# Optimization experiments

Measured on AMD Instinct MI355X. Metric: run time of the kernel, lower is better.

Reference implementation:

```python
import jax, jax.numpy as jnp
import numpy as np

N_SAMPLES = 16384
IN_FEATURES = 2048
N_COMPONENTS = 512
MAX_CROSS_TERMS = 512
# With n_components=512, max_cross_terms=512: interaction_depth=2 -> only pairwise
# cross terms, and n_pairwise = min(512*511//2, 512) = 512 (the first 512 pairs in
# lexicographic (i, j), i<j order -- exactly what the chunked torch loops produce).
_pi, _pj = np.triu_indices(N_COMPONENTS, k=1)  # lexicographic row-major order
PAIR_I = jnp.asarray(_pi[:MAX_CROSS_TERMS])
PAIR_J = jnp.asarray(_pj[:MAX_CROSS_TERMS])
SQRT_EPS = 1e-8


def setup_inputs() -> dict:
    key = jax.random.key(0)
    k1, k2 = jax.random.split(key)
    X = jax.random.normal(k1, (N_SAMPLES, IN_FEATURES), dtype=jnp.float32)
    projection = jax.random.normal(k2, (IN_FEATURES, N_COMPONENTS), dtype=jnp.float32) / np.sqrt(N_COMPONENTS)
    return {"X": X, "projection": projection}


def reference(X, projection):
    # Random projection: [N, in] @ [in, C] -> [N, C]
    Xp = X @ projection
    n = X.shape[0]
    bias = jnp.ones((n, 1), dtype=X.dtype)                 # 'bias' chunk
    p1 = Xp                                                # power_1
    p2 = Xp * Xp                                           # power_2
    p3 = p2 * Xp                                           # power_3
    pairs = Xp[:, PAIR_I] * Xp[:, PAIR_J]                  # pairwise cross terms
    sq = jnp.sqrt(jnp.abs(Xp) + SQRT_EPS)                  # sqrt features
    # Feature layout matches torch offsets: bias | p1 | p2 | p3 | cross | sqrt
    return jnp.concatenate([bias, p1, p2, p3, pairs, sq], axis=1)  # [N, 2561]
```

## Files before the change

kernel.cpp:

```cpp
#include <hip/hip_runtime.h>
#include <math.h>


typedef __attribute__((ext_vector_type(4))) float f32x4;
typedef __attribute__((ext_vector_type(8))) short bf16x8;
typedef __attribute__((ext_vector_type(4))) short s16x4;

#define MM 16384
#define NN 512
#define KK 2048
#define OUTW 2561

#define BM 64
#define BK 32
#define NT (KK / BK)

__device__ __forceinline__ short f2bf(float x) {
  union { float f; unsigned u; } c; c.f = x;
  unsigned r = c.u + 0x7fffu + ((c.u >> 16) & 1u);
  return (short)(r >> 16);
}

__device__ __forceinline__ void gl_lds16(const void* g, void* l) {
  __builtin_amdgcn_global_load_lds((const __attribute__((address_space(1))) unsigned int*)g,
                                   (__attribute__((address_space(3))) unsigned int*)l, 16, 0, 0);
}

__global__ __launch_bounds__(256) void prep_b(const float* __restrict__ P, short* __restrict__ Bt) {
  __shared__ float ts[64][65];
  const int tid = threadIdx.x;
  const int k0 = (blockIdx.x >> 3) * 64;
  const int n0 = (blockIdx.x & 7) * 64;
#pragma unroll
  for (int j = 0; j < 16; ++j) {
    int idx = j * 256 + tid;
    int kr = idx >> 6, nc = idx & 63;
    ts[kr][nc] = P[(size_t)(k0 + kr) * NN + n0 + nc];
  }
  __syncthreads();
#pragma unroll
  for (int j = 0; j < 16; ++j) {
    int idx = j * 256 + tid;
    int nr = idx >> 6, kc = idx & 63;
    Bt[(size_t)(n0 + nr) * KK + k0 + kc] = f2bf(ts[kc][nr]);
  }
}

__global__ __launch_bounds__(512) void fused_k(const float* __restrict__ X,
                                               const short* __restrict__ Bt,
                                               float* __restrict__ out) {
  __shared__ short As[2][BM * BK];
  __shared__ short Bs[2][NN * BK];
  __shared__ float s012[3][BM];

  const int tid = threadIdx.x;
  const int wid = tid >> 6, lane = tid & 63;
  const int lrow = lane & 15, kh = lane >> 4;
  const int m0 = blockIdx.x * BM;

  const int arow = tid >> 3, akq = tid & 7;
  const int aoff = arow * 32 + ((((akq >> 1)) ^ ((arow >> 1) & 3)) << 3) + (akq & 1) * 4;
  const float* aG = X + (size_t)(m0 + arow) * KK + akq * 4;

  const int kd = (lane & 3) ^ ((lane >> 3) & 3);
  const short* bG[4];
  int bOff[4];
#pragma unroll
  for (int p = 0; p < 4; ++p) {
    int nbase = (p * 8 + wid) * 16;
    bOff[p] = nbase * 32;
    bG[p] = Bt + (size_t)(nbase + (lane >> 2)) * KK + kd * 8;
  }

  f32x4 acc[4][4];
#pragma unroll
  for (int m = 0; m < 4; ++m)
#pragma unroll
    for (int n = 0; n < 4; ++n) acc[m][n] = (f32x4)0.0f;

  f32x4 aR = *(const f32x4*)aG;
#pragma unroll
  for (int p = 0; p < 4; ++p) gl_lds16(bG[p], &Bs[0][bOff[p]]);
  {
    s16x4 h;
    h[0] = f2bf(aR[0]); h[1] = f2bf(aR[1]); h[2] = f2bf(aR[2]); h[3] = f2bf(aR[3]);
    *(s16x4*)&As[0][aoff] = h;
  }
  aR = *(const f32x4*)(aG + BK);
  __syncthreads();

  int cur = 0;
  for (int t = 0; t < NT; ++t) {
    if (t + 1 < NT) {
#pragma unroll
      for (int p = 0; p < 4; ++p) gl_lds16(bG[p] + (size_t)(t + 1) * BK, &Bs[cur ^ 1][bOff[p]]);
      s16x4 h;
      h[0] = f2bf(aR[0]); h[1] = f2bf(aR[1]); h[2] = f2bf(aR[2]); h[3] = f2bf(aR[3]);
      *(s16x4*)&As[cur ^ 1][aoff] = h;
      int t2 = (t + 2 < NT) ? t + 2 : t;
      aR = *(const f32x4*)(aG + (size_t)t2 * BK);
    }
    bf16x8 af[4], bfr[4];
#pragma unroll
    for (int m = 0; m < 4; ++m) {
      int r = m * 16 + lrow;
      af[m] = *(const bf16x8*)&As[cur][r * 32 + ((kh ^ ((r >> 1) & 3)) << 3)];
    }
#pragma unroll
    for (int n = 0; n < 4; ++n) {
      int r = wid * 64 + n * 16 + lrow;
      bfr[n] = *(const bf16x8*)&Bs[cur][r * 32 + ((kh ^ ((r >> 1) & 3)) << 3)];
    }
#pragma unroll
    for (int m = 0; m < 4; ++m)
#pragma unroll
      for (int n = 0; n < 4; ++n)
        acc[m][n] = __builtin_amdgcn_mfma_f32_16x16x32_bf16(af[m], bfr[n], acc[m][n], 0, 0, 0);
    __syncthreads();
    cur ^= 1;
  }

  if (wid == 0 && lrow < 3) {
#pragma unroll
    for (int m = 0; m < 4; ++m)
#pragma unroll
      for (int r = 0; r < 4; ++r)
        s012[lrow][m * 16 + kh * 4 + r] = acc[m][0][r];
  }
  __syncthreads();

#pragma unroll
  for (int m = 0; m < 4; ++m) {
#pragma unroll
    for (int n = 0; n < 4; ++n) {
      int c = wid * 64 + n * 16 + lrow;
#pragma unroll
      for (int r = 0; r < 4; ++r) {
        int rl = m * 16 + kh * 4 + r;
        float xp = acc[m][n][r];
        float* rp = out + (size_t)(m0 + rl) * OUTW;
        float p2 = xp * xp;
        rp[1 + c] = xp;
        rp[513 + c] = p2;
        rp[1025 + c] = p2 * xp;
        rp[2049 + c] = sqrtf(fabsf(xp) + 1e-8f);
        if (c == 0) {
          rp[0] = 1.0f;
          rp[1537 + 511] = s012[1][rl] * s012[2][rl];
        } else {
          rp[1537 + c - 1] = s012[0][rl] * xp;
        }
      }
    }
  }
}

#define FBM 128
#define FBN 128
#define FBK 32
#define FPAD 40

__global__ __launch_bounds__(256) void gemm_k(const float* __restrict__ A,
                                              const float* __restrict__ B,
                                              float* __restrict__ out) {
  __shared__ __align__(16) short Asf[FBM][FPAD];
  __shared__ __align__(16) short Bsf[FBN][FPAD];
  const int tid = threadIdx.x;
  const int bx = blockIdx.x;
  const int m0 = (bx >> 2) * FBM;
  const int n0 = (bx & 3) * FBN;
  const int wid = tid >> 6, lane = tid & 63;
  const int wr = wid >> 1, wc = wid & 1;
  const int lrow = lane & 15, kh = lane >> 4;
  f32x4 acc[4][4];
#pragma unroll
  for (int i = 0; i < 4; i++)
#pragma unroll
    for (int j = 0; j < 4; j++) acc[i][j] = (f32x4)0.0f;
  for (int k0 = 0; k0 < KK; k0 += FBK) {
#pragma unroll
    for (int i = 0; i < 4; i++) {
      int fid = i * 256 + tid;
      int ar = fid >> 3, ac = (fid & 7) << 2;
      f32x4 v = *(const f32x4*)(A + (size_t)(m0 + ar) * KK + (k0 + ac));
      s16x4 h;
      h[0] = f2bf(v[0]); h[1] = f2bf(v[1]); h[2] = f2bf(v[2]); h[3] = f2bf(v[3]);
      *(s16x4*)&Asf[ar][ac] = h;
    }
#pragma unroll
    for (int i = 0; i < 4; i++) {
      int fid = i * 256 + tid;
      int br = fid >> 5, bc = (fid & 31) << 2;
      f32x4 v = *(const f32x4*)(B + (size_t)(k0 + br) * NN + (n0 + bc));
#pragma unroll
      for (int j = 0; j < 4; j++) Bsf[bc + j][br] = f2bf(v[j]);
    }
    __syncthreads();
    bf16x8 af[4], bf[4];
#pragma unroll
    for (int m = 0; m < 4; m++) af[m] = *(const bf16x8*)&Asf[wr * 64 + m * 16 + lrow][kh * 8];
#pragma unroll
    for (int n = 0; n < 4; n++) bf[n] = *(const bf16x8*)&Bsf[wc * 64 + n * 16 + lrow][kh * 8];
#pragma unroll
    for (int m = 0; m < 4; m++)
#pragma unroll
      for (int n = 0; n < 4; n++)
        acc[m][n] = __builtin_amdgcn_mfma_f32_16x16x32_bf16(af[m], bf[n], acc[m][n], 0, 0, 0);
    __syncthreads();
  }
#pragma unroll
  for (int m = 0; m < 4; m++)
#pragma unroll
    for (int n = 0; n < 4; n++)
#pragma unroll
      for (int r = 0; r < 4; r++) {
        int row = m0 + wr * 64 + m * 16 + kh * 4 + r;
        int col = n0 + wc * 64 + n * 16 + lrow;
        out[(size_t)row * OUTW + 1 + col] = acc[m][n][r];
      }
}

__global__ __launch_bounds__(512) void epi_k(float* __restrict__ out) {
  const int r = blockIdx.x;
  const int c = threadIdx.x;
  float* row = out + (size_t)r * OUTW;
  __shared__ float s[NN];
  float xp = row[1 + c];
  s[c] = xp;
  __syncthreads();
  float p2 = xp * xp;
  float p3 = p2 * xp;
  float sq = sqrtf(fabsf(xp) + 1e-8f);
  float pr = (c < 511) ? s[0] * s[c + 1] : s[1] * s[2];
  if (c == 0) row[0] = 1.0f;
  row[513 + c] = p2;
  row[1025 + c] = p3;
  row[1537 + c] = pr;
  row[2049 + c] = sq;
}

extern "C" void kernel_launch(void* const* d_in, const int* in_sizes, int n_in,
                              void* d_out, int out_size, void* d_ws, size_t ws_size,
                              hipStream_t stream) {
  const float* X = (const float*)d_in[0];
  const float* P = (const float*)d_in[1];
  float* out = (float*)d_out;
  (void)in_sizes; (void)n_in; (void)out_size;

  if (ws_size >= (size_t)NN * KK * sizeof(short)) {
    short* Bt = (short*)d_ws;
    prep_b<<<dim3(256), dim3(256), 0, stream>>>(P, Bt);
    fused_k<<<dim3(MM / BM), dim3(512), 0, stream>>>(X, Bt, out);
  } else {
    gemm_k<<<dim3(512), dim3(256), 0, stream>>>(X, P, out);
    epi_k<<<dim3(MM), dim3(512), 0, stream>>>(out);
  }
}
```

Measured before the change: 128.1 us.

## Split fused GEMM+epilogue into 64x128 tiled GEMM plus separate epilogue kernel

The fused kernel, where one block of 512 threads covered all 512 output columns for 64 rows, is replaced. The GEMM now uses 64x128 tiles with 256 threads and a swizzled block-to-tile mapping, giving 4x more blocks and a smaller LDS footprint per block. The elementwise epilogue now always runs as a separate epi_k pass that reads Xp back from the output. This buys occupancy and parallelism but writes Xp and re-reads it from global memory, and X is re-read once for each of the 4 column tiles.

```diff
diff --git a/kernel.cpp b/kernel.cpp
--- a/kernel.cpp
+++ b/kernel.cpp
@@ -1,10 +1,10 @@
 #include <hip/hip_runtime.h>
+#include <hip/hip_bf16.h>
 #include <math.h>
 
 
 typedef __attribute__((ext_vector_type(4))) float f32x4;
 typedef __attribute__((ext_vector_type(8))) short bf16x8;
-typedef __attribute__((ext_vector_type(4))) short s16x4;
 
 #define MM 16384
 #define NN 512
@@ -12,13 +12,21 @@
 #define OUTW 2561
 
 #define BM 64
+#define BN 128
 #define BK 32
 #define NT (KK / BK)
 
 __device__ __forceinline__ short f2bf(float x) {
-  union { float f; unsigned u; } c; c.f = x;
-  unsigned r = c.u + 0x7fffu + ((c.u >> 16) & 1u);
-  return (short)(r >> 16);
+  union { __hip_bfloat16 b; short s; } u;
+  u.b = __float2bfloat16(x);
+  return u.s;
+}
+
+__device__ __forceinline__ bf16x8 cvt8(f32x4 a, f32x4 b) {
+  bf16x8 r;
+  r[0] = f2bf(a[0]); r[1] = f2bf(a[1]); r[2] = f2bf(a[2]); r[3] = f2bf(a[3]);
+  r[4] = f2bf(b[0]); r[5] = f2bf(b[1]); r[6] = f2bf(b[2]); r[7] = f2bf(b[3]);
+  return r;
 }
 
 __device__ __forceinline__ void gl_lds16(const void* g, void* l) {
@@ -46,73 +54,75 @@
   }
 }
 
-__global__ __launch_bounds__(512) void fused_k(const float* __restrict__ X,
-                                               const short* __restrict__ Bt,
-                                               float* __restrict__ out) {
+__global__ __launch_bounds__(256) void gemm3(const float* __restrict__ X,
+                                             const short* __restrict__ Bt,
+                                             float* __restrict__ out) {
   __shared__ short As[2][BM * BK];
-  __shared__ short Bs[2][NN * BK];
-  __shared__ float s012[3][BM];
+  __shared__ short Bs[2][BN * BK];
 
   const int tid = threadIdx.x;
   const int wid = tid >> 6, lane = tid & 63;
   const int lrow = lane & 15, kh = lane >> 4;
-  const int m0 = blockIdx.x * BM;
-
-  const int arow = tid >> 3, akq = tid & 7;
-  const int aoff = arow * 32 + ((((akq >> 1)) ^ ((arow >> 1) & 3)) << 3) + (akq & 1) * 4;
-  const float* aG = X + (size_t)(m0 + arow) * KK + akq * 4;
+  const int wr = wid >> 1, wc = wid & 1;
+
+  const int bid = blockIdx.x;
+  const int tile = (bid & 7) * 128 + (bid >> 3);
+  const int m0 = (tile >> 2) * BM;
+  const int n0 = (tile & 3) * BN;
+
+  const int arow = tid >> 2, akq = tid & 3;
+  const float* aG = X + (size_t)(m0 + arow) * KK + akq * 8;
+  const int aoff = arow * 32 + ((akq ^ ((arow >> 1) & 3)) << 3);
 
   const int kd = (lane & 3) ^ ((lane >> 3) & 3);
-  const short* bG[4];
-  int bOff[4];
-#pragma unroll
-  for (int p = 0; p < 4; ++p) {
-    int nbase = (p * 8 + wid) * 16;
-    bOff[p] = nbase * 32;
-    bG[p] = Bt + (size_t)(nbase + (lane >> 2)) * KK + kd * 8;
-  }
-
-  f32x4 acc[4][4];
-#pragma unroll
-  for (int m = 0; m < 4; ++m)
+  const short* bG[2];
+  int bOff[2];
+#pragma unroll
+  for (int p = 0; p < 2; ++p) {
+    int R0 = (p * 4 + wid) * 16;
+    bOff[p] = R0 * 32;
+    bG[p] = Bt + (size_t)(n0 + R0 + (lane >> 2)) * KK + kd * 8;
+  }
+
+  f32x4 acc[2][4];
+#pragma unroll
+  for (int m = 0; m < 2; ++m)
 #pragma unroll
     for (int n = 0; n < 4; ++n) acc[m][n] = (f32x4)0.0f;
 
-  f32x4 aR = *(const f32x4*)aG;
-#pragma unroll
-  for (int p = 0; p < 4; ++p) gl_lds16(bG[p], &Bs[0][bOff[p]]);
-  {
-    s16x4 h;
-    h[0] = f2bf(aR[0]); h[1] = f2bf(aR[1]); h[2] = f2bf(aR[2]); h[3] = f2bf(aR[3]);
-    *(s16x4*)&As[0][aoff] = h;
-  }
-  aR = *(const f32x4*)(aG + BK);
+#pragma unroll
+  for (int p = 0; p < 2; ++p) gl_lds16(bG[p], &Bs[0][bOff[p]]);
+  f32x4 a0 = *(const f32x4*)aG;
+  f32x4 a1 = *(const f32x4*)(aG + 4);
+  *(bf16x8*)&As[0][aoff] = cvt8(a0, a1);
+  a0 = *(const f32x4*)(aG + BK);
+  a1 = *(const f32x4*)(aG + BK + 4);
   __syncthreads();
 
   int cur = 0;
   for (int t = 0; t < NT; ++t) {
     if (t + 1 < NT) {
 #pragma unroll
-      for (int p = 0; p < 4; ++p) gl_lds16(bG[p] + (size_t)(t + 1) * BK, &Bs[cur ^ 1][bOff[p]]);
-      s16x4 h;
-      h[0] = f2bf(aR[0]); h[1] = f2bf(aR[1]); h[2] = f2bf(aR[2]); h[3] = f2bf(aR[3]);
-      *(s16x4*)&As[cur ^ 1][aoff] = h;
+      for (int p = 0; p < 2; ++p) gl_lds16(bG[p] + (size_t)(t + 1) * BK, &Bs[cur ^ 1][bOff[p]]);
+      *(bf16x8*)&As[cur ^ 1][aoff] = cvt8(a0, a1);
       int t2 = (t + 2 < NT) ? t + 2 : t;
-      aR = *(const f32x4*)(aG + (size_t)t2 * BK);
-    }
-    bf16x8 af[4], bfr[4];
-#pragma unroll
-    for (int m = 0; m < 4; ++m) {
-      int r = m * 16 + lrow;
-      af[m] = *(const bf16x8*)&As[cur][r * 32 + ((kh ^ ((r >> 1) & 3)) << 3)];
+      a0 = *(const f32x4*)(aG + (size_t)t2 * BK);
+      a1 = *(const f32x4*)(aG + (size_t)t2 * BK + 4);
+    }
+    const int sw = ((lrow >> 1) & 3);
+    bf16x8 af[2], bfr[4];
+#pragma unroll
+    for (int m = 0; m < 2; ++m) {
+      int r = wr * 32 + m * 16 + lrow;
+      af[m] = *(const bf16x8*)&As[cur][r * 32 + ((kh ^ sw) << 3)];
     }
 #pragma unroll
     for (int n = 0; n < 4; ++n) {
-      int r = wid * 64 + n * 16 + lrow;
-      bfr[n] = *(const bf16x8*)&Bs[cur][r * 32 + ((kh ^ ((r >> 1) & 3)) << 3)];
-    }
-#pragma unroll
-    for (int m = 0; m < 4; ++m)
+      int r = wc * 64 + n * 16 + lrow;
+      bfr[n] = *(const bf16x8*)&Bs[cur][r * 32 + ((kh ^ sw) << 3)];
+    }
+#pragma unroll
+    for (int m = 0; m < 2; ++m)
 #pragma unroll
       for (int n = 0; n < 4; ++n)
         acc[m][n] = __builtin_amdgcn_mfma_f32_16x16x32_bf16(af[m], bfr[n], acc[m][n], 0, 0, 0);
@@ -120,101 +130,13 @@
     cur ^= 1;
   }
 
-  if (wid == 0 && lrow < 3) {
-#pragma unroll
-    for (int m = 0; m < 4; ++m)
-#pragma unroll
-      for (int r = 0; r < 4; ++r)
-        s012[lrow][m * 16 + kh * 4 + r] = acc[m][0][r];
-  }
-  __syncthreads();
-
-#pragma unroll
-  for (int m = 0; m < 4; ++m) {
-#pragma unroll
-    for (int n = 0; n < 4; ++n) {
-      int c = wid * 64 + n * 16 + lrow;
+#pragma unroll
+  for (int m = 0; m < 2; ++m)
+#pragma unroll
+    for (int n = 0; n < 4; ++n)
 #pragma unroll
       for (int r = 0; r < 4; ++r) {
-        int rl = m * 16 + kh * 4 + r;
-        float xp = acc[m][n][r];
-        float* rp = out + (size_t)(m0 + rl) * OUTW;
-        float p2 = xp * xp;
-        rp[1 + c] = xp;
-        rp[513 + c] = p2;
-        rp[1025 + c] = p2 * xp;
-        rp[2049 + c] = sqrtf(fabsf(xp) + 1e-8f);
-        if (c == 0) {
-          rp[0] = 1.0f;
-          rp[1537 + 511] = s012[1][rl] * s012[2][rl];
-        } else {
-          rp[1537 + c - 1] = s012[0][rl] * xp;
-        }
-      }
-    }
-  }
-}
-
-#define FBM 128
-#define FBN 128
-#define FBK 32
-#define FPAD 40
-
-__global__ __launch_bounds__(256) void gemm_k(const float* __restrict__ A,
-                                              const float* __restrict__ B,
-                                              float* __restrict__ out) {
-  __shared__ __align__(16) short Asf[FBM][FPAD];
-  __shared__ __align__(16) short Bsf[FBN][FPAD];
-  const int tid = threadIdx.x;
-  const int bx = blockIdx.x;
-  const int m0 = (bx >> 2) * FBM;
-  const int n0 = (bx & 3) * FBN;
-  const int wid = tid >> 6, lane = tid & 63;
-  const int wr = wid >> 1, wc = wid & 1;
-  const int lrow = lane & 15, kh = lane >> 4;
-  f32x4 acc[4][4];
-#pragma unroll
-  for (int i = 0; i < 4; i++)
-#pragma unroll
-    for (int j = 0; j < 4; j++) acc[i][j] = (f32x4)0.0f;
-  for (int k0 = 0; k0 < KK; k0 += FBK) {
-#pragma unroll
-    for (int i = 0; i < 4; i++) {
-      int fid = i * 256 + tid;
-      int ar = fid >> 3, ac = (fid & 7) << 2;
-      f32x4 v = *(const f32x4*)(A + (size_t)(m0 + ar) * KK + (k0 + ac));
-      s16x4 h;
-      h[0] = f2bf(v[0]); h[1] = f2bf(v[1]); h[2] = f2bf(v[2]); h[3] = f2bf(v[3]);
-      *(s16x4*)&Asf[ar][ac] = h;
-    }
-#pragma unroll
-    for (int i = 0; i < 4; i++) {
-      int fid = i * 256 + tid;
-      int br = fid >> 5, bc = (fid & 31) << 2;
-      f32x4 v = *(const f32x4*)(B + (size_t)(k0 + br) * NN + (n0 + bc));
-#pragma unroll
-      for (int j = 0; j < 4; j++) Bsf[bc + j][br] = f2bf(v[j]);
-    }
-    __syncthreads();
-    bf16x8 af[4], bf[4];
-#pragma unroll
-    for (int m = 0; m < 4; m++) af[m] = *(const bf16x8*)&Asf[wr * 64 + m * 16 + lrow][kh * 8];
-#pragma unroll
-    for (int n = 0; n < 4; n++) bf[n] = *(const bf16x8*)&Bsf[wc * 64 + n * 16 + lrow][kh * 8];
-#pragma unroll
-    for (int m = 0; m < 4; m++)
-#pragma unroll
-      for (int n = 0; n < 4; n++)
-        acc[m][n] = __builtin_amdgcn_mfma_f32_16x16x32_bf16(af[m], bf[n], acc[m][n], 0, 0, 0);
-    __syncthreads();
-  }
-#pragma unroll
-  for (int m = 0; m < 4; m++)
-#pragma unroll
-    for (int n = 0; n < 4; n++)
-#pragma unroll
-      for (int r = 0; r < 4; r++) {
-        int row = m0 + wr * 64 + m * 16 + kh * 4 + r;
+        int row = m0 + wr * 32 + m * 16 + kh * 4 + r;
         int col = n0 + wc * 64 + n * 16 + lrow;
         out[(size_t)row * OUTW + 1 + col] = acc[m][n][r];
       }
@@ -239,6 +161,69 @@
   row[2049 + c] = sq;
 }
 
+#define FBM 128
+#define FBN 128
+#define FPAD 40
+
+__global__ __launch_bounds__(256) void gemm_k(const float* __restrict__ A,
+                                              const float* __restrict__ B,
+                                              float* __restrict__ out) {
+  __shared__ __align__(16) short Asf[FBM][FPAD];
+  __shared__ __align__(16) short Bsf[FBN][FPAD];
+  const int tid = threadIdx.x;
+  const int bx = blockIdx.x;
+  const int m0 = (bx >> 2) * FBM;
+  const int n0 = (bx & 3) * FBN;
+  const int wid = tid >> 6, lane = tid & 63;
+  const int wr = wid >> 1, wc = wid & 1;
+  const int lrow = lane & 15, kh = lane >> 4;
+  f32x4 acc[4][4];
+#pragma unroll
+  for (int i = 0; i < 4; i++)
+#pragma unroll
+    for (int j = 0; j < 4; j++) acc[i][j] = (f32x4)0.0f;
+  for (int k0 = 0; k0 < KK; k0 += BK) {
+#pragma unroll
+    for (int i = 0; i < 4; i++) {
+      int fid = i * 256 + tid;
+      int ar = fid >> 3, ac = (fid & 7) << 2;
+      f32x4 v = *(const f32x4*)(A + (size_t)(m0 + ar) * KK + (k0 + ac));
+      short h0 = f2bf(v[0]), h1 = f2bf(v[1]), h2 = f2bf(v[2]), h3 = f2bf(v[3]);
+      Asf[ar][ac] = h0; Asf[ar][ac + 1] = h1; Asf[ar][ac + 2] = h2; Asf[ar][ac + 3] = h3;
+    }
+#pragma unroll
+    for (int i = 0; i < 4; i++) {
+      int fid = i * 256 + tid;
+      int br = fid >> 5, bc = (fid & 31) << 2;
+      f32x4 v = *(const f32x4*)(B + (size_t)(k0 + br) * NN + (n0 + bc));
+#pragma unroll
+      for (int j = 0; j < 4; j++) Bsf[bc + j][br] = f2bf(v[j]);
+    }
+    __syncthreads();
+    bf16x8 af[4], bf[4];
+#pragma unroll
+    for (int m = 0; m < 4; m++) af[m] = *(const bf16x8*)&Asf[wr * 64 + m * 16 + lrow][kh * 8];
+#pragma unroll
+    for (int n = 0; n < 4; n++) bf[n] = *(const bf16x8*)&Bsf[wc * 64 + n * 16 + lrow][kh * 8];
+#pragma unroll
+    for (int m = 0; m < 4; m++)
+#pragma unroll
+      for (int n = 0; n < 4; n++)
+        acc[m][n] = __builtin_amdgcn_mfma_f32_16x16x32_bf16(af[m], bf[n], acc[m][n], 0, 0, 0);
+    __syncthreads();
+  }
+#pragma unroll
+  for (int m = 0; m < 4; m++)
+#pragma unroll
+    for (int n = 0; n < 4; n++)
+#pragma unroll
+      for (int r = 0; r < 4; r++) {
+        int row = m0 + wr * 64 + m * 16 + kh * 4 + r;
+        int col = n0 + wc * 64 + n * 16 + lrow;
+        out[(size_t)row * OUTW + 1 + col] = acc[m][n][r];
+      }
+}
+
 extern "C" void kernel_launch(void* const* d_in, const int* in_sizes, int n_in,
                               void* d_out, int out_size, void* d_ws, size_t ws_size,
                               hipStream_t stream) {
@@ -250,9 +235,9 @@
   if (ws_size >= (size_t)NN * KK * sizeof(short)) {
     short* Bt = (short*)d_ws;
     prep_b<<<dim3(256), dim3(256), 0, stream>>>(P, Bt);
-    fused_k<<<dim3(MM / BM), dim3(512), 0, stream>>>(X, Bt, out);
+    gemm3<<<dim3((MM / BM) * (NN / BN)), dim3(256), 0, stream>>>(X, Bt, out);
   } else {
     gemm_k<<<dim3(512), dim3(256), 0, stream>>>(X, P, out);
-    epi_k<<<dim3(MM), dim3(512), 0, stream>>>(out);
-  }
-}
+  }
+  epi_k<<<dim3(MM), dim3(512), 0, stream>>>(out);
+}
```

After: 138.5 us. +8.1%, slower.
